# Performance work log

Measured on AMD Instinct MI355X. Metric: run time of the kernel, lower is better.

## Reference

```python
import jax, jax.numpy as jnp
import numpy as np

B, IN, OUT, T = 64, 1024, 512, 512
V_TH = 1.0
TAU = 16.0


def alpha_kernel(t, tau):
    # SRM alpha kernel: (t/tau)*exp(1 - t/tau) for t > 0, else 0.
    # Mask BEFORE exp to avoid overflow for large negative t.
    ts = jnp.where(t > 0, t, tau)
    v = (ts / tau) * jnp.exp(1.0 - ts / tau)
    return jnp.where(t > 0, v, 0.0)


def setup_inputs() -> dict:
    key = jax.random.key(0)
    k1, k2 = jax.random.split(key)
    # input spike times in [0, T/2)
    in_spike = jax.random.uniform(k1, (B, IN), dtype=jnp.float32) * (T / 2)
    weight = jax.random.normal(k2, (OUT, IN), dtype=jnp.float32) / np.float32(np.sqrt(IN))
    return {"in_spike": in_spike, "weight": weight}


def reference(in_spike, weight):
    t_seq = jnp.arange(T, dtype=jnp.float32)                  # [T]
    time_sequence = t_seq[None, None, :] - in_spike[:, :, None]  # [B, in, T]
    v_input = alpha_kernel(time_sequence, TAU)                 # [B, in, T]
    # fc applied along the `in` axis at every time step
    membrane_voltage = jnp.einsum('bit,oi->bot', v_input, weight)  # [B, out, T]
    # first time index where voltage crosses threshold; T if never.
    mask = membrane_voltage >= V_TH                            # [B, out, T]
    spiked = mask.any(axis=-1)
    first_t = jnp.argmax(mask, axis=-1)                        # first True index
    out_spike = jnp.where(spiked, first_t, T).astype(jnp.float32)  # [B, out]
    return out_spike
```

## Files before the change

kernel.cpp:

```cpp
#include <hip/hip_runtime.h>
#include <math.h>

#define BATCH   64
#define INS     1024
#define OUTS    512
#define TSTEPS  512
#define TAUF    16.0f
#define LOG2E_OVER_TAU 0.0901684400555602f

#define TT 64
#define NTRANS ((INS / TT) * (OUTS / TT))

__global__ __launch_bounds__(256) void pre_kernel(
        const float* __restrict__ w, float* __restrict__ wT,
        const float* __restrict__ in_spike, float4* __restrict__ spk,
        int* __restrict__ starts) {
    __shared__ float tile[TT][TT + 1];
    __shared__ int hist[257];
    __shared__ int cursor[257];
    __shared__ int wsum[4];

    if (blockIdx.x < NTRANS) {
        const int i0 = (blockIdx.x & (INS / TT - 1)) * TT;
        const int o0 = (blockIdx.x / (INS / TT)) * TT;
        const int c  = threadIdx.x & 63;
        const int r  = threadIdx.x >> 6;
#pragma unroll
        for (int rr = r; rr < TT; rr += 4)
            tile[rr][c] = w[(o0 + rr) * INS + i0 + c];
        __syncthreads();
#pragma unroll
        for (int rr = r; rr < TT; rr += 4)
            wT[(i0 + rr) * OUTS + o0 + c] = tile[c][rr];
        return;
    }

    const int b = blockIdx.x - NTRANS;
    const int tid = threadIdx.x;
    for (int k = tid; k < 257; k += 256) hist[k] = 0;
    __syncthreads();

    float sv[INS / 256];
    int   tv[INS / 256];
#pragma unroll
    for (int j = 0; j < INS / 256; ++j) {
        int i = tid + j * 256;
        float s = in_spike[b * INS + i];
        sv[j] = s;
        int t = (int)floorf(s) + 1;
        t = t < 1 ? 1 : (t > 256 ? 256 : t);
        tv[j] = t;
        atomicAdd(&hist[t], 1);
    }
    __syncthreads();

    const int lane = tid & 63;
    const int wv   = tid >> 6;
    int v = hist[tid + 1];
    int sc = v;
#pragma unroll
    for (int off = 1; off < 64; off <<= 1) {
        int n = __shfl_up(sc, off, 64);
        if (lane >= off) sc += n;
    }
    if (lane == 63) wsum[wv] = sc;
    __syncthreads();
    int base = 0;
    for (int j = 0; j < wv; ++j) base += wsum[j];
    int excl = sc + base - v;
    cursor[tid + 1] = excl;
    starts[b * 258 + tid + 1] = excl;
    if (tid == 0) { starts[b * 258] = 0; starts[b * 258 + 257] = INS; }
    __syncthreads();

#pragma unroll
    for (int j = 0; j < INS / 256; ++j) {
        int i = tid + j * 256;
        int t = tv[j];
        int pos = atomicAdd(&cursor[t], 1);
        float A = expf(fmaf(sv[j], 1.0f / TAUF, 1.0f)) * (1.0f / TAUF);
        float C = -sv[j] * A;
        spk[b * INS + pos] =
            make_float4(A, __int_as_float(i * (OUTS / 2)), C, __int_as_float(t));
    }
}

#define OL 32
#define G  32
#define WS 8
#define TAIL0 257

__global__ __launch_bounds__(OL * G, 8) void spike_scan_kernel(
        const float4* __restrict__ spk, const int* __restrict__ starts,
        const float* __restrict__ wT, float* __restrict__ out) {
    const int b = blockIdx.x;
    const int x = threadIdx.x;
    const int g = threadIdx.y;
    const int tid = g * OL + x;

    __shared__ float4 sspk[INS];
    __shared__ float2 psP0[G][OL];
    __shared__ float2 psP1[G][OL];
    __shared__ int    sSt[258];
    __shared__ int    sFirst[2 * OL];

    sspk[tid] = spk[b * INS + tid];
    if (tid < 258) sSt[tid] = starts[b * 258 + tid];
    if (tid < 2 * OL) sFirst[tid] = TSTEPS;
    __syncthreads();

    const int w0 = g * WS + 1;
    const float2* __restrict__ wT2x = (const float2*)wT + (blockIdx.y * OL + x);

    float cA0 = 0.f, cC0 = 0.f, cA1 = 0.f, cC1 = 0.f;
    float l00, l01, l02, l03, l04, l05, l06, l07;
    float l10, l11, l12, l13, l14, l15, l16, l17;
    int k = sSt[w0];

#define BUCKET(D, LA, LB)                                                     \
    {                                                                         \
        const int e = sSt[w0 + (D) + 1];                                      \
        for (; k + 2 <= e; k += 2) {                                          \
            float4 p0 = sspk[k + 0];                                          \
            float4 p1 = sspk[k + 1];                                          \
            float2 q0 = wT2x[__float_as_int(p0.y)];                           \
            float2 q1 = wT2x[__float_as_int(p1.y)];                           \
            cA0 = fmaf(q0.x, p0.x, cA0); cC0 = fmaf(q0.x, p0.z, cC0);         \
            cA1 = fmaf(q0.y, p0.x, cA1); cC1 = fmaf(q0.y, p0.z, cC1);         \
            cA0 = fmaf(q1.x, p1.x, cA0); cC0 = fmaf(q1.x, p1.z, cC0);         \
            cA1 = fmaf(q1.y, p1.x, cA1); cC1 = fmaf(q1.y, p1.z, cC1);         \
        }                                                                     \
        if (k < e) {                                                          \
            float4 p = sspk[k];                                               \
            float2 q = wT2x[__float_as_int(p.y)];                             \
            cA0 = fmaf(q.x, p.x, cA0); cC0 = fmaf(q.x, p.z, cC0);             \
            cA1 = fmaf(q.y, p.x, cA1); cC1 = fmaf(q.y, p.z, cC1);             \
            ++k;                                                              \
        }                                                                     \
        const float tf = (float)(w0 + (D));                                   \
        LA = fmaf(tf, cA0, cC0);                                              \
        LB = fmaf(tf, cA1, cC1);                                              \
    }

    BUCKET(0, l00, l10)
    BUCKET(1, l01, l11)
    BUCKET(2, l02, l12)
    BUCKET(3, l03, l13)
    BUCKET(4, l04, l14)
    BUCKET(5, l05, l15)
    BUCKET(6, l06, l16)
    BUCKET(7, l07, l17)
#undef BUCKET

    psP0[g][x] = make_float2(cA0, cC0);
    psP1[g][x] = make_float2(cA1, cC1);
    __syncthreads();

    float SA0 = 0.f, SC0 = 0.f, SA1 = 0.f, SC1 = 0.f;
    for (int j = 0; j < g; ++j) {
        float2 a = psP0[j][x];
        float2 c = psP1[j][x];
        SA0 += a.x; SC0 += a.y; SA1 += c.x; SC1 += c.y;
    }
    float TA0 = SA0, TC0 = SC0, TA1 = SA1, TC1 = SC1;
    for (int j = g; j < G; ++j) {
        float2 a = psP0[j][x];
        float2 c = psP1[j][x];
        TA0 += a.x; TC0 += a.y; TA1 += c.x; TC1 += c.y;
    }

    unsigned m0 = 0, m1 = 0;
#define CHECK(D, LA, LB)                                                      \
    {                                                                         \
        const float tf = (float)(w0 + (D));                                   \
        const float ev = exp2f(tf * LOG2E_OVER_TAU);                          \
        m0 |= (fmaf(tf, SA0, SC0) + (LA) >= ev) ? (1u << (D)) : 0u;           \
        m1 |= (fmaf(tf, SA1, SC1) + (LB) >= ev) ? (1u << (D)) : 0u;           \
    }
    CHECK(0, l00, l10)
    CHECK(1, l01, l11)
    CHECK(2, l02, l12)
    CHECK(3, l03, l13)
    CHECK(4, l04, l14)
    CHECK(5, l05, l15)
    CHECK(6, l06, l16)
    CHECK(7, l07, l17)
#undef CHECK
    int f0 = m0 ? (w0 + __builtin_ffs(m0) - 1) : TSTEPS;
    int f1 = m1 ? (w0 + __builtin_ffs(m1) - 1) : TSTEPS;

    {
        const int t0 = TAIL0 + g * WS;
        unsigned n0 = 0, n1 = 0;
        float tg = (float)t0;
        for (int d = 0; d < WS; ++d) {
            if (t0 + d < TSTEPS) {
                float ev = exp2f(tg * LOG2E_OVER_TAU);
                n0 |= (fmaf(tg, TA0, TC0) >= ev) ? (1u << d) : 0u;
                n1 |= (fmaf(tg, TA1, TC1) >= ev) ? (1u << d) : 0u;
            }
            tg += 1.0f;
        }
        if (n0) f0 = min(f0, t0 + __builtin_ffs(n0) - 1);
        if (n1) f1 = min(f1, t0 + __builtin_ffs(n1) - 1);
    }

    if (f0 < TSTEPS) atomicMin(&sFirst[2 * x], f0);
    if (f1 < TSTEPS) atomicMin(&sFirst[2 * x + 1], f1);
    __syncthreads();
    if (tid < 2 * OL)
        out[b * OUTS + blockIdx.y * (2 * OL) + tid] = (float)sFirst[tid];
}

extern "C" void kernel_launch(void* const* d_in, const int* in_sizes, int n_in,
                              void* d_out, int out_size, void* d_ws, size_t ws_size,
                              hipStream_t stream) {
    const float* in_spike = (const float*)d_in[0];
    const float* weight   = (const float*)d_in[1];
    float* out = (float*)d_out;

    float*  wT     = (float*)d_ws;
    float4* spk    = (float4*)((char*)d_ws + (size_t)INS * OUTS * sizeof(float));
    int*    starts = (int*)((char*)d_ws + (size_t)INS * OUTS * sizeof(float)
                                        + (size_t)BATCH * INS * sizeof(float4));

    pre_kernel<<<NTRANS + BATCH, 256, 0, stream>>>(weight, wT, in_spike, spk, starts);
    spike_scan_kernel<<<dim3(BATCH, OUTS / (2 * OL)), dim3(OL, G), 0, stream>>>(
        spk, starts, wT, out);
}
```

Before: 81.36 us.

## Use direct global-to-LDS load, byte-offset weight addressing, two-level prefix sum

Stages the per-batch spike records into shared memory with the global_load_lds builtin instead of going through registers. The gather index is prescaled to a byte offset in the pre kernel, and a 32-bit lane offset is added to it, which trims address arithmetic in the inner loop. The linear prefix sum over 32 groups becomes a two-level scan of 8-group segments plus a small segment-totals array, at the cost of an extra barrier. The global_load_lds builtin needs hardware support for 16-byte transfers and correct ordering before the barrier.

```diff
diff --git a/kernel.cpp b/kernel.cpp
--- a/kernel.cpp
+++ b/kernel.cpp
@@ -81,7 +81,7 @@
         float A = expf(fmaf(sv[j], 1.0f / TAUF, 1.0f)) * (1.0f / TAUF);
         float C = -sv[j] * A;
         spk[b * INS + pos] =
-            make_float4(A, __int_as_float(i * (OUTS / 2)), C, __int_as_float(t));
+            make_float4(A, __int_as_float(i * (OUTS * 4)), C, __int_as_float(t));
     }
 }
 
@@ -89,6 +89,10 @@
 #define G  32
 #define WS 8
 #define TAIL0 257
+#define NGRP 8
+#define NG (G / NGRP)
+
+typedef unsigned int u32;
 
 __global__ __launch_bounds__(OL * G, 8) void spike_scan_kernel(
         const float4* __restrict__ spk, const int* __restrict__ starts,
@@ -99,18 +103,25 @@
     const int tid = g * OL + x;
 
     __shared__ float4 sspk[INS];
-    __shared__ float2 psP0[G][OL];
-    __shared__ float2 psP1[G][OL];
+    __shared__ float4 sP[G][OL];
+    __shared__ float4 sQ[NG][OL];
     __shared__ int    sSt[258];
     __shared__ int    sFirst[2 * OL];
 
-    sspk[tid] = spk[b * INS + tid];
+    {
+        auto gsrc = (const __attribute__((address_space(1))) u32*)
+                        (spk + (size_t)b * INS + tid);
+        auto ldst = (__attribute__((address_space(3))) u32*)&sspk[tid];
+        __builtin_amdgcn_global_load_lds(gsrc, ldst, 16, 0, 0);
+    }
     if (tid < 258) sSt[tid] = starts[b * 258 + tid];
     if (tid < 2 * OL) sFirst[tid] = TSTEPS;
     __syncthreads();
 
     const int w0 = g * WS + 1;
-    const float2* __restrict__ wT2x = (const float2*)wT + (blockIdx.y * OL + x);
+    const char* __restrict__ wTb =
+        (const char*)wT + ((size_t)blockIdx.y * OL) * sizeof(float2);
+    const u32 x8 = (u32)(x << 3);
 
     float cA0 = 0.f, cC0 = 0.f, cA1 = 0.f, cC1 = 0.f;
     float l00, l01, l02, l03, l04, l05, l06, l07;
@@ -123,8 +134,8 @@
         for (; k + 2 <= e; k += 2) {                                          \
             float4 p0 = sspk[k + 0];                                          \
             float4 p1 = sspk[k + 1];                                          \
-            float2 q0 = wT2x[__float_as_int(p0.y)];                           \
-            float2 q1 = wT2x[__float_as_int(p1.y)];                           \
+            float2 q0 = *(const float2*)(wTb + ((u32)__float_as_int(p0.y) + x8)); \
+            float2 q1 = *(const float2*)(wTb + ((u32)__float_as_int(p1.y) + x8)); \
             cA0 = fmaf(q0.x, p0.x, cA0); cC0 = fmaf(q0.x, p0.z, cC0);         \
             cA1 = fmaf(q0.y, p0.x, cA1); cC1 = fmaf(q0.y, p0.z, cC1);         \
             cA0 = fmaf(q1.x, p1.x, cA0); cC0 = fmaf(q1.x, p1.z, cC0);         \
@@ -132,7 +143,7 @@
         }                                                                     \
         if (k < e) {                                                          \
             float4 p = sspk[k];                                               \
-            float2 q = wT2x[__float_as_int(p.y)];                             \
+            float2 q = *(const float2*)(wTb + ((u32)__float_as_int(p.y) + x8)); \
             cA0 = fmaf(q.x, p.x, cA0); cC0 = fmaf(q.x, p.z, cC0);             \
             cA1 = fmaf(q.y, p.x, cA1); cC1 = fmaf(q.y, p.z, cC1);             \
             ++k;                                                              \
@@ -152,21 +163,31 @@
     BUCKET(7, l07, l17)
 #undef BUCKET
 
-    psP0[g][x] = make_float2(cA0, cC0);
-    psP1[g][x] = make_float2(cA1, cC1);
+    sP[g][x] = make_float4(cA0, cC0, cA1, cC1);
     __syncthreads();
 
     float SA0 = 0.f, SC0 = 0.f, SA1 = 0.f, SC1 = 0.f;
-    for (int j = 0; j < g; ++j) {
-        float2 a = psP0[j][x];
-        float2 c = psP1[j][x];
-        SA0 += a.x; SC0 += a.y; SA1 += c.x; SC1 += c.y;
-    }
-    float TA0 = SA0, TC0 = SC0, TA1 = SA1, TC1 = SC1;
-    for (int j = g; j < G; ++j) {
-        float2 a = psP0[j][x];
-        float2 c = psP1[j][x];
-        TA0 += a.x; TC0 += a.y; TA1 += c.x; TC1 += c.y;
+    {
+        const int g0 = g & ~(NGRP - 1);
+        for (int j = g0; j < g; ++j) {
+            float4 v = sP[j][x];
+            SA0 += v.x; SC0 += v.y; SA1 += v.z; SC1 += v.w;
+        }
+    }
+    if ((g & (NGRP - 1)) == (NGRP - 1))
+        sQ[g >> 3][x] = make_float4(SA0 + cA0, SC0 + cC0, SA1 + cA1, SC1 + cC1);
+    __syncthreads();
+    float TA0 = 0.f, TC0 = 0.f, TA1 = 0.f, TC1 = 0.f;
+    {
+        const int myg = g >> 3;
+#pragma unroll
+        for (int s = 0; s < NG; ++s) {
+            float4 qv = sQ[s][x];
+            TA0 += qv.x; TC0 += qv.y; TA1 += qv.z; TC1 += qv.w;
+            if (s < myg) {
+                SA0 += qv.x; SC0 += qv.y; SA1 += qv.z; SC1 += qv.w;
+            }
+        }
     }
 
     unsigned m0 = 0, m1 = 0;
```

New measurement: 93.15 us. 14.5% more time.
